# Performance work log

Hardware: AMD Instinct MI355X
Metric: run time of the kernel (lower is better)

## Reference

```python
import jax, jax.numpy as jnp
import numpy as np

# Hyperparameters from __init__
TEMPERATURE = 0.07
HARD_POS_W = 1.5
HARD_NEG_W = 2.0
THR_POS = 0.5
THR_NEG = 0.3
NEG_LOSS_W = 0.3

B, D, N_CLASSES = 8192, 256, 1024


def setup_inputs() -> dict:
    key = jax.random.key(0)
    kf, kl = jax.random.split(key)
    features = jax.random.normal(kf, (B, D), dtype=jnp.float32)
    labels = jax.random.randint(kl, (B,), 0, N_CLASSES, dtype=jnp.int32)
    return {"features": features, "labels": labels}


def reference(features, labels):
    b = features.shape[0]
    # L2-normalize features (F.normalize(dim=1))
    anchor = features / jnp.linalg.norm(features, axis=1, keepdims=True)
    sim = anchor @ anchor.T                      # [B, B] cosine similarity
    logits = sim / TEMPERATURE
    logits = logits - jax.lax.stop_gradient(jnp.max(logits, axis=1, keepdims=True))

    mask = (labels[:, None] == labels[None, :]).astype(logits.dtype)   # same-class
    logits_mask = 1.0 - jnp.eye(b, dtype=logits.dtype)                 # exclude self

    # W2ML weights: computed from detached similarities (torch used .item())
    sim_d = jax.lax.stop_gradient(sim)
    offdiag = logits_mask > 0
    is_pos = mask > 0
    hard_pos = is_pos & (sim_d < THR_POS) & offdiag
    pos_weights = jnp.where(
        hard_pos, 1.0 + (THR_POS - sim_d) / THR_POS * (HARD_POS_W - 1.0), 1.0)
    hard_neg = (~is_pos) & (sim_d > THR_NEG) & offdiag
    neg_weights = jnp.where(
        hard_neg, 1.0 + (sim_d - THR_NEG) / (1.0 - THR_NEG) * (HARD_NEG_W - 1.0), 1.0)

    # SupCon log-prob with self excluded from the denominator
    exp_logits = jnp.exp(logits) * logits_mask
    denom = jnp.sum(exp_logits, axis=1, keepdims=True)
    log_prob = logits - jnp.log(denom)

    pos_mask = mask * logits_mask
    pos_cnt = jnp.clip(jnp.sum(pos_mask, axis=1), 1.0, None)
    positive_loss = -jnp.mean(
        jnp.sum(pos_mask * pos_weights * log_prob, axis=1) / pos_cnt)

    # Negative term: weighted mean probability mass assigned to negatives
    neg_mask = (1.0 - mask) * logits_mask
    neg_cnt = jnp.clip(jnp.sum(neg_mask, axis=1), 1.0, None)
    prob = exp_logits / denom
    negative_loss = jnp.mean(
        jnp.sum(neg_mask * neg_weights * prob, axis=1) / neg_cnt)

    return positive_loss + NEG_LOSS_W * negative_loss
```

## Files before the change

kernel.cpp:

```cpp
#include <hip/hip_runtime.h>

#define BSZ  8192
#define DDIM 256
#define BM 128
#define BN 128
#define NT   64
#define NTRI (NT * (NT + 1) / 2)

typedef float f32x4 __attribute__((ext_vector_type(4)));
typedef short bf16x8 __attribute__((ext_vector_type(8)));

__device__ __forceinline__ unsigned short f32_to_bf16(float f) {
    unsigned int u = __float_as_uint(f);
    u += 0x7fffu + ((u >> 16) & 1u);
    return (unsigned short)(u >> 16);
}

#if __has_builtin(__builtin_amdgcn_exp2f)
__device__ __forceinline__ float fast_exp2(float x) { return __builtin_amdgcn_exp2f(x); }
#else
__device__ __forceinline__ float fast_exp2(float x) {
    float r;
    asm("v_exp_f32 %0, %1" : "=v"(r) : "v"(x));
    return r;
}
#endif

#define K_E1   20.60992915555662f
#define K_E2  -20.60992915555662f
#define K_INVT 14.285714285714286f
#define K_N1   1.4285714285714286f
#define K_N2   0.5714285714285714f

__device__ __forceinline__ void decode_tile(int t, int& It, int& Jt) {
    const int off1 = 136, off2 = 392, off3 = 648, off4 = 904, off5 = 1040,
              off6 = 1296, off7 = 1552, off8 = 1688, off9 = 1944;
    int b = (t >= off1) + (t >= off2) + (t >= off3) + (t >= off4) + (t >= off5)
          + (t >= off6) + (t >= off7) + (t >= off8) + (t >= off9);
    int si, sj, r0;
    switch (b) {
        case 0: si = 0; sj = 0; r0 = 0;    break;
        case 1: si = 0; sj = 1; r0 = off1; break;
        case 2: si = 0; sj = 2; r0 = off2; break;
        case 3: si = 0; sj = 3; r0 = off3; break;
        case 4: si = 1; sj = 1; r0 = off4; break;
        case 5: si = 1; sj = 2; r0 = off5; break;
        case 6: si = 1; sj = 3; r0 = off6; break;
        case 7: si = 2; sj = 2; r0 = off7; break;
        case 8: si = 2; sj = 3; r0 = off8; break;
        default: si = 3; sj = 3; r0 = off9; break;
    }
    const int rr = t - r0;
    int il, jl;
    if (si == sj) {
        il = 0;
        #pragma unroll
        for (int q = 1; q < 16; q++) if (rr >= (16 * q - (q * (q - 1)) / 2)) il = q;
        jl = il + (rr - (16 * il - (il * (il - 1)) / 2));
    } else {
        il = rr >> 4;
        jl = rr & 15;
    }
    It = si * 16 + il;
    Jt = sj * 16 + jl;
}

__global__ __launch_bounds__(256) void norm_kernel(const float* __restrict__ feat,
                                                   unsigned short* __restrict__ anchorT,
                                                   float* __restrict__ posAcc,
                                                   unsigned int* __restrict__ counter) {
    __shared__ __align__(16) unsigned short img[8 * 512];
    const int tid  = threadIdx.x;
    const int wid  = tid >> 6;
    const int lane = tid & 63;
    const int R    = blockIdx.x;
    const int R0   = R * 16;

    if (tid < 64) posAcc[blockIdx.x * 64 + tid] = 0.0f;
    if (blockIdx.x == 0 && tid == 0) *counter = 0u;

    #pragma unroll
    for (int it = 0; it < 4; it++) {
        const int row = R0 + it * 4 + wid;
        const float4 v = ((const float4*)(feat + (size_t)row * DDIM))[lane];
        float ss = v.x * v.x + v.y * v.y + v.z * v.z + v.w * v.w;
        #pragma unroll
        for (int off = 32; off > 0; off >>= 1) ss += __shfl_xor(ss, off, 64);
        const float inv = rsqrtf(ss);
        ushort4 o;
        o.x = f32_to_bf16(v.x * inv);
        o.y = f32_to_bf16(v.y * inv);
        o.z = f32_to_bf16(v.z * inv);
        o.w = f32_to_bf16(v.w * inv);
        const int C    = lane >> 3;
        const int l16  = (row & 15) + (((lane >> 1) & 3) << 4);
        *(ushort4*)(&img[C * 512 + l16 * 8 + (lane & 1) * 4]) = o;
    }
    __syncthreads();
    #pragma unroll
    for (int p = 0; p < 2; p++) {
        const int c = p * 4 + wid;
        *(bf16x8*)(anchorT + ((size_t)(c * 512 + R)) * 512 + lane * 8) =
            *(const bf16x8*)(&img[c * 512 + lane * 8]);
    }
}

__device__ __forceinline__ void gload_lds16(const unsigned short* g, unsigned short* l) {
    __builtin_amdgcn_global_load_lds(
        (const __attribute__((address_space(1))) void*)g,
        (__attribute__((address_space(3))) void*)l, 16, 0, 0);
}

__global__ __launch_bounds__(512) void simloss_kernel(
    const unsigned short* __restrict__ anchorT,
    const int* __restrict__ labels,
    float* __restrict__ part,
    float* __restrict__ posAcc)
{
    __shared__ __align__(16) unsigned short As[8 * 512];
    __shared__ __align__(16) unsigned short As2[8 * 512];
    __shared__ __align__(16) unsigned short Bs[8 * 512];
    __shared__ __align__(16) unsigned short Bs2[8 * 512];
    __shared__ float rowDT[2][BM][2];
    __shared__ float colDT[4][BN][2];
    __shared__ int rowLab[BM];
    __shared__ int colLab[BN];

    int It, Jt;
    decode_tile(blockIdx.x, It, Jt);
    const bool diag = (It == Jt);
    const int I0 = It * BM, J0 = Jt * BN;

    const int tid  = threadIdx.x;
    const int lane = tid & 63;
    const int w    = tid >> 6;
    const int rw   = w >> 1;
    const int cw   = w & 1;
    const int cl   = lane & 15;
    const int rg   = lane >> 4;
    const int laneOff = lane * 8;

    if (tid < BM) rowLab[tid] = labels[I0 + tid];
    else if (tid < 2 * BM) colLab[tid - BM] = labels[J0 + tid - BM];

    f32x4 acc[2][4];
    #pragma unroll
    for (int f = 0; f < 2; f++)
        #pragma unroll
        for (int g = 0; g < 4; g++)
            acc[f][g] = (f32x4){0.f, 0.f, 0.f, 0.f};

    #pragma unroll
    for (int kc = 0; kc < 4; kc++) {
        {
            const int C0 = kc * 2;
            const size_t ga0 = ((size_t)C0 * 512 + It * 8) * 512;
            const size_t gb0 = ((size_t)C0 * 512 + Jt * 8) * 512;
            const size_t ga1 = ((size_t)(C0 + 1) * 512 + It * 8) * 512;
            const size_t gb1 = ((size_t)(C0 + 1) * 512 + Jt * 8) * 512;
            gload_lds16(anchorT + ga0 + tid * 8, &As[w * 512]);
            gload_lds16(anchorT + gb0 + tid * 8, &Bs[w * 512]);
            gload_lds16(anchorT + ga1 + tid * 8, &As2[w * 512]);
            gload_lds16(anchorT + gb1 + tid * 8, &Bs2[w * 512]);
        }
        __syncthreads();
        #pragma unroll
        for (int ks = 0; ks < 2; ks++) {
            const unsigned short* aB = (ks == 0 ? As : As2) + (rw * 2) * 512 + laneOff;
            const unsigned short* bB = (ks == 0 ? Bs : Bs2) + (cw * 4) * 512 + laneOff;
            const bf16x8 a0 = *(const bf16x8*)(aB);
            const bf16x8 a1 = *(const bf16x8*)(aB + 512);
            const bf16x8 b0 = *(const bf16x8*)(bB);
            const bf16x8 b1 = *(const bf16x8*)(bB + 512);
            const bf16x8 b2 = *(const bf16x8*)(bB + 1024);
            const bf16x8 b3 = *(const bf16x8*)(bB + 1536);
            acc[0][0] = __builtin_amdgcn_mfma_f32_16x16x32_bf16(a0, b0, acc[0][0], 0, 0, 0);
            acc[0][1] = __builtin_amdgcn_mfma_f32_16x16x32_bf16(a0, b1, acc[0][1], 0, 0, 0);
            acc[0][2] = __builtin_amdgcn_mfma_f32_16x16x32_bf16(a0, b2, acc[0][2], 0, 0, 0);
            acc[0][3] = __builtin_amdgcn_mfma_f32_16x16x32_bf16(a0, b3, acc[0][3], 0, 0, 0);
            acc[1][0] = __builtin_amdgcn_mfma_f32_16x16x32_bf16(a1, b0, acc[1][0], 0, 0, 0);
            acc[1][1] = __builtin_amdgcn_mfma_f32_16x16x32_bf16(a1, b1, acc[1][1], 0, 0, 0);
            acc[1][2] = __builtin_amdgcn_mfma_f32_16x16x32_bf16(a1, b2, acc[1][2], 0, 0, 0);
            acc[1][3] = __builtin_amdgcn_mfma_f32_16x16x32_bf16(a1, b3, acc[1][3], 0, 0, 0);
        }
        __syncthreads();
    }

    int ljr[4], gjr[4];
    #pragma unroll
    for (int g = 0; g < 4; g++) {
        const int cidx = cw * 64 + g * 16 + cl;
        ljr[g] = colLab[cidx];
        gjr[g] = J0 + cidx;
    }
    float cd[4] = {0.f, 0.f, 0.f, 0.f}, ct[4] = {0.f, 0.f, 0.f, 0.f};

    #pragma unroll
    for (int f = 0; f < 2; f++) {
        float rd[4] = {0.f, 0.f, 0.f, 0.f}, rt[4] = {0.f, 0.f, 0.f, 0.f};
        int li[4], gi[4];
        #pragma unroll
        for (int r = 0; r < 4; r++) {
            const int ridx = rw * 32 + f * 16 + rg * 4 + r;
            li[r] = rowLab[ridx];
            gi[r] = I0 + ridx;
        }
        #pragma unroll
        for (int g = 0; g < 4; g++) {
            const int lj = ljr[g];
            const bool granule = (rw * 2 + f) == (cw * 4 + g);
            const f32x4 c = acc[f][g];
            #pragma unroll
            for (int r = 0; r < 4; r++) {
                const float s = c[r];
                const bool self = diag && granule && ((rg * 4 + r) == cl);
                const float e  = self ? 0.f : fast_exp2(fmaf(s, K_E1, K_E2));
                const float wn = fmaxf(fmaf(s, K_N1, K_N2), 1.0f);
                const float we = wn * e;
                rd[r] += e;  rt[r] += we;
                if (!diag) { cd[g] += e; ct[g] += we; }
                if (li[r] == lj && !self) {
                    const float wp = fmaxf(1.5f - s, 1.0f);
                    const float slp = fmaf(s, K_INVT, -K_INVT) * wp;
                    float* pi = posAcc + (size_t)gi[r] * 4;
                    atomicAdd(pi + 0, slp);
                    atomicAdd(pi + 1, wp);
                    atomicAdd(pi + 2, we);
                    atomicAdd(pi + 3, 1.0f);
                    if (!diag) {
                        float* pj = posAcc + (size_t)gjr[g] * 4;
                        atomicAdd(pj + 0, slp);
                        atomicAdd(pj + 1, wp);
                        atomicAdd(pj + 2, we);
                        atomicAdd(pj + 3, 1.0f);
                    }
                }
            }
        }
        #pragma unroll
        for (int r = 0; r < 4; r++) {
            #pragma unroll
            for (int off = 1; off < 16; off <<= 1) {
                rd[r] += __shfl_xor(rd[r], off, 64);
                rt[r] += __shfl_xor(rt[r], off, 64);
            }
        }
        if (cl == 0) {
            #pragma unroll
            for (int r = 0; r < 4; r++) {
                const int row = rw * 32 + f * 16 + rg * 4 + r;
                rowDT[cw][row][0] = rd[r];
                rowDT[cw][row][1] = rt[r];
            }
        }
    }
    if (!diag) {
        #pragma unroll
        for (int g = 0; g < 4; g++) {
            cd[g] += __shfl_xor(cd[g], 16, 64);
            cd[g] += __shfl_xor(cd[g], 32, 64);
            ct[g] += __shfl_xor(ct[g], 16, 64);
            ct[g] += __shfl_xor(ct[g], 32, 64);
        }
        if (rg == 0) {
            #pragma unroll
            for (int g = 0; g < 4; g++) {
                const int col = cw * 64 + g * 16 + cl;
                colDT[rw][col][0] = cd[g];
                colDT[rw][col][1] = ct[g];
            }
        }
    }

    __syncthreads();
    if (tid < BM) {
        float2 v;
        v.x = rowDT[0][tid][0] + rowDT[1][tid][0];
        v.y = rowDT[0][tid][1] + rowDT[1][tid][1];
        ((float2*)part)[(size_t)Jt * BSZ + I0 + tid] = v;
    } else if (tid < 2 * BM && !diag) {
        const int c = tid - BM;
        float2 v;
        v.x = colDT[0][c][0] + colDT[1][c][0] + colDT[2][c][0] + colDT[3][c][0];
        v.y = colDT[0][c][1] + colDT[1][c][1] + colDT[2][c][1] + colDT[3][c][1];
        ((float2*)part)[(size_t)It * BSZ + J0 + c] = v;
    }
}

__global__ __launch_bounds__(256) void reduce_final_kernel(
    const float* __restrict__ part, const float* __restrict__ posAcc,
    double* __restrict__ partial, unsigned int* __restrict__ counter,
    float* __restrict__ out)
{
    const int t   = threadIdx.x;
    const int row = blockIdx.x * 32 + (t >> 3);
    const int sg  = t & 7;
    float dsum = 0.f, T2 = 0.f;
    const float2* p2 = (const float2*)part;
    #pragma unroll
    for (int j = 0; j < 8; j++) {
        const float2 v = p2[(size_t)(sg * 8 + j) * BSZ + row];
        dsum += v.x; T2 += v.y;
    }
    #pragma unroll
    for (int off = 1; off < 8; off <<= 1) {
        dsum += __shfl_xor(dsum, off, 64);
        T2   += __shfl_xor(T2,   off, 64);
    }
    __shared__ double sp[32], sn[32];
    if (sg == 0) {
        const float4 pa = ((const float4*)posAcc)[row];
        const float s1 = pa.x, w1 = pa.y, s2 = T2 - pa.z, cnt = pa.w;
        const float pc = fmaxf(cnt, 1.0f);
        const float nc = fmaxf(8191.0f - cnt, 1.0f);
        const float ld = logf(dsum);
        sp[t >> 3] = (double)((s1 - ld * w1) / pc);
        sn[t >> 3] = (double)((s2 / dsum) / nc);
    }
    __syncthreads();
    __shared__ bool amLast;
    if (t < 32) {
        double p = sp[t], n = sn[t];
        #pragma unroll
        for (int off = 1; off < 32; off <<= 1) {
            p += __shfl_xor(p, off, 64);
            n += __shfl_xor(n, off, 64);
        }
        if (t == 0) {
            partial[blockIdx.x * 2 + 0] = p;
            partial[blockIdx.x * 2 + 1] = n;
            __threadfence();
            amLast = (atomicAdd(counter, 1u) == 255u);
        }
    }
    __syncthreads();
    if (amLast) {
        __threadfence();
        __shared__ double fp[256], fn[256];
        volatile double* vp = (volatile double*)partial;
        fp[t] = vp[t * 2 + 0];
        fn[t] = vp[t * 2 + 1];
        __syncthreads();
        for (int s = 128; s > 0; s >>= 1) {
            if (t < s) { fp[t] += fp[t + s]; fn[t] += fn[t + s]; }
            __syncthreads();
        }
        if (t == 0) out[0] = (float)(-fp[0] / (double)BSZ + 0.3 * (fn[0] / (double)BSZ));
    }
}

extern "C" void kernel_launch(void* const* d_in, const int* in_sizes, int n_in,
                              void* d_out, int out_size, void* d_ws, size_t ws_size,
                              hipStream_t stream) {
    const float* feat = (const float*)d_in[0];
    const int* labels = (const int*)d_in[1];
    float* out = (float*)d_out;

    char* ws = (char*)d_ws;
    unsigned short* anchorT = (unsigned short*)ws;
    const size_t anchorBytes = (size_t)BSZ * DDIM * sizeof(unsigned short);
    float* part = (float*)(ws + anchorBytes);
    const size_t partBytes = (size_t)NT * BSZ * 2 * sizeof(float);
    float* posAcc = (float*)(ws + anchorBytes + partBytes);
    const size_t posBytes = (size_t)BSZ * 4 * sizeof(float);
    double* partial = (double*)(ws + anchorBytes + partBytes + posBytes);
    unsigned int* counter = (unsigned int*)(ws + anchorBytes + partBytes + posBytes + 4096);

    norm_kernel<<<BSZ / 16, 256, 0, stream>>>(feat, anchorT, posAcc, counter);
    simloss_kernel<<<NTRI, 512, 0, stream>>>(anchorT, labels, part, posAcc);
    reduce_final_kernel<<<BSZ / 32, 256, 0, stream>>>(part, posAcc, partial, counter, out);
}
```

Before: 117.2 us.

## Fuse final reduction into simloss via atomic row accumulation and last-block finish

Replaces the per-tile partial buffer and separate reduce kernel with float atomicAdd of row/column sums into a compact per-row accumulator. The last simloss block, detected with a global counter, computes the final loss over all 8192 rows. This removes one kernel launch and the large partial-buffer traffic, but adds atomic contention and a serial tail where a single block reduces every row. It also switches the fast hardware exp2 intrinsic back to exp2f, which may cost extra instructions in the epilogue, and float atomics make the summation order nondeterministic.

```diff
diff --git a/kernel.cpp b/kernel.cpp
--- a/kernel.cpp
+++ b/kernel.cpp
@@ -15,16 +15,6 @@
     u += 0x7fffu + ((u >> 16) & 1u);
     return (unsigned short)(u >> 16);
 }
-
-#if __has_builtin(__builtin_amdgcn_exp2f)
-__device__ __forceinline__ float fast_exp2(float x) { return __builtin_amdgcn_exp2f(x); }
-#else
-__device__ __forceinline__ float fast_exp2(float x) {
-    float r;
-    asm("v_exp_f32 %0, %1" : "=v"(r) : "v"(x));
-    return r;
-}
-#endif
 
 #define K_E1   20.60992915555662f
 #define K_E2  -20.60992915555662f
@@ -67,6 +57,7 @@
 
 __global__ __launch_bounds__(256) void norm_kernel(const float* __restrict__ feat,
                                                    unsigned short* __restrict__ anchorT,
+                                                   float* __restrict__ acc,
                                                    float* __restrict__ posAcc,
                                                    unsigned int* __restrict__ counter) {
     __shared__ __align__(16) unsigned short img[8 * 512];
@@ -77,6 +68,7 @@
     const int R0   = R * 16;
 
     if (tid < 64) posAcc[blockIdx.x * 64 + tid] = 0.0f;
+    if (tid < 32) acc[blockIdx.x * 32 + tid] = 0.0f;
     if (blockIdx.x == 0 && tid == 0) *counter = 0u;
 
     #pragma unroll
@@ -114,8 +106,10 @@
 __global__ __launch_bounds__(512) void simloss_kernel(
     const unsigned short* __restrict__ anchorT,
     const int* __restrict__ labels,
-    float* __restrict__ part,
-    float* __restrict__ posAcc)
+    float* __restrict__ acc,
+    float* __restrict__ posAcc,
+    unsigned int* __restrict__ counter,
+    float* __restrict__ out)
 {
     __shared__ __align__(16) unsigned short As[8 * 512];
     __shared__ __align__(16) unsigned short As2[8 * 512];
@@ -143,12 +137,12 @@
     if (tid < BM) rowLab[tid] = labels[I0 + tid];
     else if (tid < 2 * BM) colLab[tid - BM] = labels[J0 + tid - BM];
 
-    f32x4 acc[2][4];
+    f32x4 acc_r[2][4];
     #pragma unroll
     for (int f = 0; f < 2; f++)
         #pragma unroll
         for (int g = 0; g < 4; g++)
-            acc[f][g] = (f32x4){0.f, 0.f, 0.f, 0.f};
+            acc_r[f][g] = (f32x4){0.f, 0.f, 0.f, 0.f};
 
     #pragma unroll
     for (int kc = 0; kc < 4; kc++) {
@@ -174,14 +168,14 @@
             const bf16x8 b1 = *(const bf16x8*)(bB + 512);
             const bf16x8 b2 = *(const bf16x8*)(bB + 1024);
             const bf16x8 b3 = *(const bf16x8*)(bB + 1536);
-            acc[0][0] = __builtin_amdgcn_mfma_f32_16x16x32_bf16(a0, b0, acc[0][0], 0, 0, 0);
-            acc[0][1] = __builtin_amdgcn_mfma_f32_16x16x32_bf16(a0, b1, acc[0][1], 0, 0, 0);
-            acc[0][2] = __builtin_amdgcn_mfma_f32_16x16x32_bf16(a0, b2, acc[0][2], 0, 0, 0);
-            acc[0][3] = __builtin_amdgcn_mfma_f32_16x16x32_bf16(a0, b3, acc[0][3], 0, 0, 0);
-            acc[1][0] = __builtin_amdgcn_mfma_f32_16x16x32_bf16(a1, b0, acc[1][0], 0, 0, 0);
-            acc[1][1] = __builtin_amdgcn_mfma_f32_16x16x32_bf16(a1, b1, acc[1][1], 0, 0, 0);
-            acc[1][2] = __builtin_amdgcn_mfma_f32_16x16x32_bf16(a1, b2, acc[1][2], 0, 0, 0);
-            acc[1][3] = __builtin_amdgcn_mfma_f32_16x16x32_bf16(a1, b3, acc[1][3], 0, 0, 0);
+            acc_r[0][0] = __builtin_amdgcn_mfma_f32_16x16x32_bf16(a0, b0, acc_r[0][0], 0, 0, 0);
+            acc_r[0][1] = __builtin_amdgcn_mfma_f32_16x16x32_bf16(a0, b1, acc_r[0][1], 0, 0, 0);
+            acc_r[0][2] = __builtin_amdgcn_mfma_f32_16x16x32_bf16(a0, b2, acc_r[0][2], 0, 0, 0);
+            acc_r[0][3] = __builtin_amdgcn_mfma_f32_16x16x32_bf16(a0, b3, acc_r[0][3], 0, 0, 0);
+            acc_r[1][0] = __builtin_amdgcn_mfma_f32_16x16x32_bf16(a1, b0, acc_r[1][0], 0, 0, 0);
+            acc_r[1][1] = __builtin_amdgcn_mfma_f32_16x16x32_bf16(a1, b1, acc_r[1][1], 0, 0, 0);
+            acc_r[1][2] = __builtin_amdgcn_mfma_f32_16x16x32_bf16(a1, b2, acc_r[1][2], 0, 0, 0);
+            acc_r[1][3] = __builtin_amdgcn_mfma_f32_16x16x32_bf16(a1, b3, acc_r[1][3], 0, 0, 0);
         }
         __syncthreads();
     }
@@ -209,12 +203,12 @@
         for (int g = 0; g < 4; g++) {
             const int lj = ljr[g];
             const bool granule = (rw * 2 + f) == (cw * 4 + g);
-            const f32x4 c = acc[f][g];
+            const f32x4 c = acc_r[f][g];
             #pragma unroll
             for (int r = 0; r < 4; r++) {
                 const float s = c[r];
                 const bool self = diag && granule && ((rg * 4 + r) == cl);
-                const float e  = self ? 0.f : fast_exp2(fmaf(s, K_E1, K_E2));
+                const float e  = self ? 0.f : exp2f(fmaf(s, K_E1, K_E2));
                 const float wn = fmaxf(fmaf(s, K_N1, K_N2), 1.0f);
                 const float we = wn * e;
                 rd[r] += e;  rt[r] += we;
@@ -274,78 +268,53 @@
 
     __syncthreads();
     if (tid < BM) {
-        float2 v;
-        v.x = rowDT[0][tid][0] + rowDT[1][tid][0];
-        v.y = rowDT[0][tid][1] + rowDT[1][tid][1];
-        ((float2*)part)[(size_t)Jt * BSZ + I0 + tid] = v;
+        float* a = acc + (size_t)(I0 + tid) * 2;
+        atomicAdd(a + 0, rowDT[0][tid][0] + rowDT[1][tid][0]);
+        atomicAdd(a + 1, rowDT[0][tid][1] + rowDT[1][tid][1]);
     } else if (tid < 2 * BM && !diag) {
         const int c = tid - BM;
-        float2 v;
-        v.x = colDT[0][c][0] + colDT[1][c][0] + colDT[2][c][0] + colDT[3][c][0];
-        v.y = colDT[0][c][1] + colDT[1][c][1] + colDT[2][c][1] + colDT[3][c][1];
-        ((float2*)part)[(size_t)It * BSZ + J0 + c] = v;
-    }
-}
-
-__global__ __launch_bounds__(256) void reduce_final_kernel(
-    const float* __restrict__ part, const float* __restrict__ posAcc,
-    double* __restrict__ partial, unsigned int* __restrict__ counter,
-    float* __restrict__ out)
-{
-    const int t   = threadIdx.x;
-    const int row = blockIdx.x * 32 + (t >> 3);
-    const int sg  = t & 7;
-    float dsum = 0.f, T2 = 0.f;
-    const float2* p2 = (const float2*)part;
-    #pragma unroll
-    for (int j = 0; j < 8; j++) {
-        const float2 v = p2[(size_t)(sg * 8 + j) * BSZ + row];
-        dsum += v.x; T2 += v.y;
-    }
-    #pragma unroll
-    for (int off = 1; off < 8; off <<= 1) {
-        dsum += __shfl_xor(dsum, off, 64);
-        T2   += __shfl_xor(T2,   off, 64);
-    }
-    __shared__ double sp[32], sn[32];
-    if (sg == 0) {
-        const float4 pa = ((const float4*)posAcc)[row];
-        const float s1 = pa.x, w1 = pa.y, s2 = T2 - pa.z, cnt = pa.w;
-        const float pc = fmaxf(cnt, 1.0f);
-        const float nc = fmaxf(8191.0f - cnt, 1.0f);
-        const float ld = logf(dsum);
-        sp[t >> 3] = (double)((s1 - ld * w1) / pc);
-        sn[t >> 3] = (double)((s2 / dsum) / nc);
-    }
+        float* a = acc + (size_t)(J0 + c) * 2;
+        atomicAdd(a + 0, colDT[0][c][0] + colDT[1][c][0] + colDT[2][c][0] + colDT[3][c][0]);
+        atomicAdd(a + 1, colDT[0][c][1] + colDT[1][c][1] + colDT[2][c][1] + colDT[3][c][1]);
+    }
+
     __syncthreads();
     __shared__ bool amLast;
-    if (t < 32) {
-        double p = sp[t], n = sn[t];
-        #pragma unroll
-        for (int off = 1; off < 32; off <<= 1) {
-            p += __shfl_xor(p, off, 64);
-            n += __shfl_xor(n, off, 64);
-        }
-        if (t == 0) {
-            partial[blockIdx.x * 2 + 0] = p;
-            partial[blockIdx.x * 2 + 1] = n;
-            __threadfence();
-            amLast = (atomicAdd(counter, 1u) == 255u);
-        }
+    if (tid == 0) {
+        __threadfence();
+        amLast = (atomicAdd(counter, 1u) == (unsigned)(NTRI - 1));
     }
     __syncthreads();
     if (amLast) {
         __threadfence();
-        __shared__ double fp[256], fn[256];
-        volatile double* vp = (volatile double*)partial;
-        fp[t] = vp[t * 2 + 0];
-        fn[t] = vp[t * 2 + 1];
+        double p = 0.0, n = 0.0;
+        for (int row = tid; row < BSZ; row += 512) {
+            volatile float* av = (volatile float*)(acc + (size_t)row * 2);
+            const float dsum = av[0];
+            const float T2   = av[1];
+            volatile float* pv = (volatile float*)(posAcc + (size_t)row * 4);
+            const float s1 = pv[0], w1 = pv[1], pcorr = pv[2], cnt = pv[3];
+            const float s2 = T2 - pcorr;
+            const float pc = fmaxf(cnt, 1.0f);
+            const float nc = fmaxf(8191.0f - cnt, 1.0f);
+            const float ld = logf(dsum);
+            p += (double)((s1 - ld * w1) / pc);
+            n += (double)((s2 / dsum) / nc);
+        }
+        #pragma unroll
+        for (int off = 32; off > 0; off >>= 1) {
+            p += __shfl_xor(p, off, 64);
+            n += __shfl_xor(n, off, 64);
+        }
+        __shared__ double sp[8], sn[8];
+        if (lane == 0) { sp[w] = p; sn[w] = n; }
         __syncthreads();
-        for (int s = 128; s > 0; s >>= 1) {
-            if (t < s) { fp[t] += fp[t + s]; fn[t] += fn[t + s]; }
-            __syncthreads();
-        }
-        if (t == 0) out[0] = (float)(-fp[0] / (double)BSZ + 0.3 * (fn[0] / (double)BSZ));
+        if (tid == 0) {
+            double P = 0.0, N = 0.0;
+            #pragma unroll
+            for (int q = 0; q < 8; q++) { P += sp[q]; N += sn[q]; }
+            out[0] = (float)(-P / (double)BSZ + 0.3 * (N / (double)BSZ));
+        }
     }
 }
 
@@ -359,14 +328,12 @@
     char* ws = (char*)d_ws;
     unsigned short* anchorT = (unsigned short*)ws;
     const size_t anchorBytes = (size_t)BSZ * DDIM * sizeof(unsigned short);
-    float* part = (float*)(ws + anchorBytes);
-    const size_t partBytes = (size_t)NT * BSZ * 2 * sizeof(float);
-    float* posAcc = (float*)(ws + anchorBytes + partBytes);
+    float* acc = (float*)(ws + anchorBytes);
+    const size_t accBytes = (size_t)BSZ * 2 * sizeof(float);
+    float* posAcc = (float*)(ws + anchorBytes + accBytes);
     const size_t posBytes = (size_t)BSZ * 4 * sizeof(float);
-    double* partial = (double*)(ws + anchorBytes + partBytes + posBytes);
-    unsigned int* counter = (unsigned int*)(ws + anchorBytes + partBytes + posBytes + 4096);
-
-    norm_kernel<<<BSZ / 16, 256, 0, stream>>>(feat, anchorT, posAcc, counter);
-    simloss_kernel<<<NTRI, 512, 0, stream>>>(anchorT, labels, part, posAcc);
-    reduce_final_kernel<<<BSZ / 32, 256, 0, stream>>>(part, posAcc, partial, counter, out);
-}
+    unsigned int* counter = (unsigned int*)(ws + anchorBytes + accBytes + posBytes);
+
+    norm_kernel<<<BSZ / 16, 256, 0, stream>>>(feat, anchorT, acc, posAcc, counter);
+    simloss_kernel<<<NTRI, 512, 0, stream>>>(anchorT, labels, acc, posAcc, counter, out);
+}
```

New measurement: 150.8 us. +28.7%, slower.
